# Kernel optimization log

Measured on AMD Instinct MI355X. Metric: run time of the kernel, lower is better.

The kernel has to match this reference:

```python
import jax, jax.numpy as jnp
import numpy as np

QMAX = 127.0  # int8 symmetric range


def _fake_quant(v, scale):
    # symmetric int8 fake-quantization with straight-through estimator
    q = jnp.round(jnp.clip(v / scale, -QMAX, QMAX)) * scale
    return v + jax.lax.stop_gradient(q - v)


def setup_inputs() -> dict:
    key = jax.random.key(0)
    k1, k2, k3 = jax.random.split(key, 3)
    B, S, Din, Dout = 4, 4096, 4096, 4096
    x = jax.random.normal(k1, (B, S, Din), dtype=jnp.float32)
    weight = jax.random.normal(k2, (Dout, Din), dtype=jnp.float32) * 0.02
    bias = jax.random.normal(k3, (Dout,), dtype=jnp.float32) * 0.02
    return {"x": x, "weight": weight, "bias": bias}


def reference(x, weight, bias):
    # per-tensor activation scale
    scale_x = jnp.maximum(jnp.max(jnp.abs(x)), 1e-8) / QMAX
    # per-output-channel weight scale: [Dout, 1]
    scale_w = jnp.maximum(jnp.max(jnp.abs(weight), axis=1, keepdims=True), 1e-8) / QMAX
    xq = _fake_quant(x, scale_x)
    wq = _fake_quant(weight, scale_w)
    # quantized linear: [B,S,Din] @ [Din,Dout] + bias
    return jnp.einsum('bsi,oi->bso', xq, wq) + bias
```

## Files before the change

kernel.cpp:

```cpp
#include <hip/hip_runtime.h>
#include <stdint.h>

#define QMAX_F 127.0f

typedef int    i32x4  __attribute__((ext_vector_type(4)));
typedef float  f32x4  __attribute__((ext_vector_type(4)));
typedef int8_t i8x16  __attribute__((ext_vector_type(16)));

#define GLOBAL_AS(p) ((const __attribute__((address_space(1))) void*)(p))
#define LDS_AS(p)    ((__attribute__((address_space(3))) void*)(p))

__global__ void init_ws_kernel(unsigned* absmax_bits) {
    if (threadIdx.x == 0) absmax_bits[0] = 0u;
}

__global__ void absmax_x_kernel(const float* __restrict__ x, size_t n4,
                                unsigned* __restrict__ out_bits) {
    size_t stride = (size_t)gridDim.x * blockDim.x;
    float m = 0.f;
    for (size_t i = (size_t)blockIdx.x * blockDim.x + threadIdx.x; i < n4; i += stride) {
        f32x4 v = reinterpret_cast<const f32x4*>(x)[i];
        m = fmaxf(m, fmaxf(fmaxf(fabsf(v[0]), fabsf(v[1])),
                           fmaxf(fabsf(v[2]), fabsf(v[3]))));
    }
    #pragma unroll
    for (int off = 32; off > 0; off >>= 1) m = fmaxf(m, __shfl_down(m, off));
    __shared__ float red[4];
    int lane = threadIdx.x & 63, wid = threadIdx.x >> 6;
    if (lane == 0) red[wid] = m;
    __syncthreads();
    if (threadIdx.x == 0) {
        m = fmaxf(fmaxf(red[0], red[1]), fmaxf(red[2], red[3]));
        atomicMax(out_bits, __float_as_uint(m));
    }
}

__global__ void rowmax_w_kernel(const float* __restrict__ w,
                                float* __restrict__ rowmax, int K) {
    int row = blockIdx.x;
    const f32x4* wr4 = reinterpret_cast<const f32x4*>(w + (size_t)row * K);
    float m = 0.f;
    for (int j = threadIdx.x; j < (K >> 2); j += blockDim.x) {
        f32x4 v = wr4[j];
        m = fmaxf(m, fmaxf(fmaxf(fabsf(v[0]), fabsf(v[1])),
                           fmaxf(fabsf(v[2]), fabsf(v[3]))));
    }
    #pragma unroll
    for (int off = 32; off > 0; off >>= 1) m = fmaxf(m, __shfl_down(m, off));
    __shared__ float red[4];
    int lane = threadIdx.x & 63, wid = threadIdx.x >> 6;
    if (lane == 0) red[wid] = m;
    __syncthreads();
    if (threadIdx.x == 0)
        rowmax[row] = fmaxf(fmaxf(red[0], red[1]), fmaxf(red[2], red[3]));
}

__global__ void quant_x_kernel(const float* __restrict__ x, int8_t* __restrict__ xq,
                               const unsigned* __restrict__ mx_bits, size_t n16) {
    float sx = fmaxf(__uint_as_float(*mx_bits), 1e-8f) / QMAX_F;
    size_t stride = (size_t)gridDim.x * blockDim.x;
    for (size_t i = (size_t)blockIdx.x * blockDim.x + threadIdx.x; i < n16; i += stride) {
        i8x16 q;
        #pragma unroll
        for (int j = 0; j < 4; ++j) {
            f32x4 v = reinterpret_cast<const f32x4*>(x)[i * 4 + j];
            #pragma unroll
            for (int k = 0; k < 4; ++k) {
                float t = fminf(fmaxf(v[k] / sx, -QMAX_F), QMAX_F);
                q[j * 4 + k] = (int8_t)__float2int_rn(t);
            }
        }
        reinterpret_cast<i8x16*>(xq)[i] = q;
    }
}

__global__ void quant_w_kernel(const float* __restrict__ w, int8_t* __restrict__ wq,
                               const float* __restrict__ rowmax,
                               float* __restrict__ scale_w, int K) {
    int row = blockIdx.x;
    float sw = fmaxf(rowmax[row], 1e-8f) / QMAX_F;
    if (threadIdx.x == 0) scale_w[row] = sw;
    const f32x4* src = reinterpret_cast<const f32x4*>(w + (size_t)row * K);
    int8_t* dst = wq + (size_t)row * K;
    for (int base = threadIdx.x * 16; base < K; base += blockDim.x * 16) {
        i8x16 q;
        #pragma unroll
        for (int j = 0; j < 4; ++j) {
            f32x4 v = src[(base >> 2) + j];
            #pragma unroll
            for (int k = 0; k < 4; ++k) {
                float t = fminf(fmaxf(v[k] / sw, -QMAX_F), QMAX_F);
                q[j * 4 + k] = (int8_t)__float2int_rn(t);
            }
        }
        *reinterpret_cast<i8x16*>(dst + base) = q;
    }
}

#define BM 128
#define BN 128
#define BKQ 64

__global__ __launch_bounds__(256) void gemm_i8_kernel(
        const int8_t* __restrict__ Aq, const int8_t* __restrict__ Bq,
        const unsigned* __restrict__ mx_bits, const float* __restrict__ scale_w,
        const float* __restrict__ bias, float* __restrict__ C,
        int M, int N, int K) {
    __shared__ __align__(16) int8_t lA[BM * BKQ];
    __shared__ __align__(16) int8_t lB[BN * BKQ];

    const int tid = threadIdx.x;
    const int l   = tid & 63;
    const int w   = tid >> 6;

    const int nwg = gridDim.x;
    const int wg  = (blockIdx.x & 7) * (nwg >> 3) + (blockIdx.x >> 3);
    const int tiles_n = N / BN;
    const int tm = wg / tiles_n, tn = wg % tiles_n;
    const size_t m0 = (size_t)tm * BM, n0 = (size_t)tn * BN;

    const int8_t* gA[2]; const int8_t* gB[2];
    const int8_t* ldsA[2]; const int8_t* ldsB[2];
    #pragma unroll
    for (int i = 0; i < 2; ++i) {
        int c   = w + 4 * i;
        int row = c * 16 + (l >> 2);
        int g   = (l & 3) ^ ((row >> 1) & 3);
        gA[i]   = Aq + (m0 + row) * (size_t)K + g * 16;
        gB[i]   = Bq + (n0 + row) * (size_t)K + g * 16;
        ldsA[i] = lA + c * 1024;
        ldsB[i] = lB + c * 1024;
    }

    const int wr = w >> 1, wc = w & 1;
    const int pbyte = (((l >> 4) ^ (((l & 15) >> 1) & 3)) << 4);
    int offA[4], offB[4];
    #pragma unroll
    for (int m = 0; m < 4; ++m) {
        offA[m] = (wr * 64 + m * 16 + (l & 15)) * BKQ + pbyte;
        offB[m] = (wc * 64 + m * 16 + (l & 15)) * BKQ + pbyte;
    }

    i32x4 acc[4][4];
    #pragma unroll
    for (int m = 0; m < 4; ++m)
        #pragma unroll
        for (int n = 0; n < 4; ++n)
            acc[m][n] = (i32x4){0, 0, 0, 0};

    for (int kt = 0; kt < K; kt += BKQ) {
        #pragma unroll
        for (int i = 0; i < 2; ++i) {
            __builtin_amdgcn_global_load_lds(GLOBAL_AS(gA[i] + kt), LDS_AS(ldsA[i]), 16, 0, 0);
            __builtin_amdgcn_global_load_lds(GLOBAL_AS(gB[i] + kt), LDS_AS(ldsB[i]), 16, 0, 0);
        }
        __syncthreads();

        i32x4 af[4], bf[4];
        #pragma unroll
        for (int m = 0; m < 4; ++m)
            af[m] = *reinterpret_cast<const i32x4*>(lA + offA[m]);
        #pragma unroll
        for (int n = 0; n < 4; ++n)
            bf[n] = *reinterpret_cast<const i32x4*>(lB + offB[n]);

        #pragma unroll
        for (int m = 0; m < 4; ++m)
            #pragma unroll
            for (int n = 0; n < 4; ++n)
                acc[m][n] = __builtin_amdgcn_mfma_i32_16x16x64_i8(af[m], bf[n], acc[m][n], 0, 0, 0);

        __syncthreads();
    }

    float sx = fmaxf(__uint_as_float(*mx_bits), 1e-8f) / QMAX_F;
    const int colb = (int)n0 + wc * 64 + (l & 15);
    const int rowb = (int)m0 + wr * 64 + ((l >> 4) << 2);
    #pragma unroll
    for (int n = 0; n < 4; ++n) {
        int col = colb + n * 16;
        float s  = sx * scale_w[col];
        float bv = bias[col];
        #pragma unroll
        for (int m = 0; m < 4; ++m) {
            size_t base = (size_t)(rowb + m * 16) * N + col;
            #pragma unroll
            for (int r = 0; r < 4; ++r)
                C[base + (size_t)r * N] = (float)acc[m][n][r] * s + bv;
        }
    }
}

extern "C" void kernel_launch(void* const* d_in, const int* in_sizes, int n_in,
                              void* d_out, int out_size, void* d_ws, size_t ws_size,
                              hipStream_t stream) {
    const float* x    = (const float*)d_in[0];
    const float* wt   = (const float*)d_in[1];
    const float* bias = (const float*)d_in[2];
    float* out        = (float*)d_out;

    const int N = in_sizes[2];
    const int K = in_sizes[1] / N;
    const int M = in_sizes[0] / K;
    const size_t nx = (size_t)in_sizes[0];
    const size_t nw = (size_t)in_sizes[1];

    uint8_t* ws = (uint8_t*)d_ws;
    unsigned* absmax_bits = (unsigned*)ws;
    float*    rowmax      = (float*)(ws + 1024);
    float*    scale_w     = (float*)(ws + 1024 + (size_t)N * 4 + 3072);
    int8_t*   xq          = (int8_t*)(ws + 65536);
    int8_t*   wq          = xq + nx;

    hipLaunchKernelGGL(init_ws_kernel, dim3(1), dim3(64), 0, stream, absmax_bits);
    hipLaunchKernelGGL(absmax_x_kernel, dim3(2048), dim3(256), 0, stream,
                       x, nx / 4, absmax_bits);
    hipLaunchKernelGGL(rowmax_w_kernel, dim3(N), dim3(256), 0, stream,
                       wt, rowmax, K);
    hipLaunchKernelGGL(quant_x_kernel, dim3(4096), dim3(256), 0, stream,
                       x, xq, absmax_bits, nx / 16);
    hipLaunchKernelGGL(quant_w_kernel, dim3(N), dim3(256), 0, stream,
                       wt, wq, rowmax, scale_w, K);

    dim3 ggrid((M / BM) * (N / BN));
    hipLaunchKernelGGL(gemm_i8_kernel, ggrid, dim3(256), 0, stream,
                       xq, wq, absmax_bits, scale_w, bias, out, M, N, K);
}
```

Before: 916.6 us.

## Rewrite int8 GEMM as double-buffered 256x256 tile pipeline and fuse weight quant

The int8 GEMM moves from 128x128 tiles with a single LDS buffer and a full barrier stall on each k-step to 256x256x128 tiles with 512 threads. It double-buffers LDS and interleaves async global-to-LDS loads with MFMA phases, using raised wave priority and partial vmcnt waits. The weight row-max and quantization kernels are merged into one pass that keeps each row in registers. The init kernel becomes a memset, and quantized outputs are packed into 32-bit words. The aim is to hide memory latency and raise arithmetic intensity, at the cost of more LDS and registers per block (launch_bounds 512,2) and a hardcoded assumption that K equals 4096 in the weight kernel.

```diff
diff --git a/kernel.cpp b/kernel.cpp
--- a/kernel.cpp
+++ b/kernel.cpp
@@ -3,16 +3,11 @@
 
 #define QMAX_F 127.0f
 
-typedef int    i32x4  __attribute__((ext_vector_type(4)));
-typedef float  f32x4  __attribute__((ext_vector_type(4)));
-typedef int8_t i8x16  __attribute__((ext_vector_type(16)));
+typedef int    i32x4 __attribute__((ext_vector_type(4)));
+typedef float  f32x4 __attribute__((ext_vector_type(4)));
 
 #define GLOBAL_AS(p) ((const __attribute__((address_space(1))) void*)(p))
 #define LDS_AS(p)    ((__attribute__((address_space(3))) void*)(p))
-
-__global__ void init_ws_kernel(unsigned* absmax_bits) {
-    if (threadIdx.x == 0) absmax_bits[0] = 0u;
-}
 
 __global__ void absmax_x_kernel(const float* __restrict__ x, size_t n4,
                                 unsigned* __restrict__ out_bits) {
@@ -35,83 +30,86 @@
     }
 }
 
-__global__ void rowmax_w_kernel(const float* __restrict__ w,
-                                float* __restrict__ rowmax, int K) {
-    int row = blockIdx.x;
-    const f32x4* wr4 = reinterpret_cast<const f32x4*>(w + (size_t)row * K);
-    float m = 0.f;
-    for (int j = threadIdx.x; j < (K >> 2); j += blockDim.x) {
-        f32x4 v = wr4[j];
-        m = fmaxf(m, fmaxf(fmaxf(fabsf(v[0]), fabsf(v[1])),
-                           fmaxf(fabsf(v[2]), fabsf(v[3]))));
-    }
-    #pragma unroll
-    for (int off = 32; off > 0; off >>= 1) m = fmaxf(m, __shfl_down(m, off));
-    __shared__ float red[4];
-    int lane = threadIdx.x & 63, wid = threadIdx.x >> 6;
-    if (lane == 0) red[wid] = m;
-    __syncthreads();
-    if (threadIdx.x == 0)
-        rowmax[row] = fmaxf(fmaxf(red[0], red[1]), fmaxf(red[2], red[3]));
-}
-
 __global__ void quant_x_kernel(const float* __restrict__ x, int8_t* __restrict__ xq,
                                const unsigned* __restrict__ mx_bits, size_t n16) {
     float sx = fmaxf(__uint_as_float(*mx_bits), 1e-8f) / QMAX_F;
     size_t stride = (size_t)gridDim.x * blockDim.x;
     for (size_t i = (size_t)blockIdx.x * blockDim.x + threadIdx.x; i < n16; i += stride) {
-        i8x16 q;
+        uint32_t q[4];
         #pragma unroll
         for (int j = 0; j < 4; ++j) {
             f32x4 v = reinterpret_cast<const f32x4*>(x)[i * 4 + j];
+            uint32_t p = 0;
             #pragma unroll
             for (int k = 0; k < 4; ++k) {
                 float t = fminf(fmaxf(v[k] / sx, -QMAX_F), QMAX_F);
-                q[j * 4 + k] = (int8_t)__float2int_rn(t);
+                p |= (uint32_t)(uint8_t)(int8_t)__float2int_rn(t) << (8 * k);
             }
+            q[j] = p;
         }
-        reinterpret_cast<i8x16*>(xq)[i] = q;
-    }
-}
-
-__global__ void quant_w_kernel(const float* __restrict__ w, int8_t* __restrict__ wq,
-                               const float* __restrict__ rowmax,
-                               float* __restrict__ scale_w, int K) {
+        reinterpret_cast<i32x4*>(xq)[i] =
+            (i32x4){(int)q[0], (int)q[1], (int)q[2], (int)q[3]};
+    }
+}
+
+__global__ __launch_bounds__(256) void wquant_kernel(const float* __restrict__ w,
+        int8_t* __restrict__ wq, float* __restrict__ scale_w, int K) {
     int row = blockIdx.x;
-    float sw = fmaxf(rowmax[row], 1e-8f) / QMAX_F;
-    if (threadIdx.x == 0) scale_w[row] = sw;
     const f32x4* src = reinterpret_cast<const f32x4*>(w + (size_t)row * K);
-    int8_t* dst = wq + (size_t)row * K;
-    for (int base = threadIdx.x * 16; base < K; base += blockDim.x * 16) {
-        i8x16 q;
+    f32x4 v[4];
+    float m = 0.f;
+    #pragma unroll
+    for (int j = 0; j < 4; ++j) {
+        v[j] = src[threadIdx.x + j * 256];
+        m = fmaxf(m, fmaxf(fmaxf(fabsf(v[j][0]), fabsf(v[j][1])),
+                           fmaxf(fabsf(v[j][2]), fabsf(v[j][3]))));
+    }
+    #pragma unroll
+    for (int off = 32; off > 0; off >>= 1) m = fmaxf(m, __shfl_down(m, off));
+    __shared__ float red[5];
+    int lane = threadIdx.x & 63, wid = threadIdx.x >> 6;
+    if (lane == 0) red[wid] = m;
+    __syncthreads();
+    if (threadIdx.x == 0) {
+        float mm = fmaxf(fmaxf(red[0], red[1]), fmaxf(red[2], red[3]));
+        float sw = fmaxf(mm, 1e-8f) / QMAX_F;
+        scale_w[row] = sw;
+        red[4] = sw;
+    }
+    __syncthreads();
+    float sw = red[4];
+    uint32_t* dst = reinterpret_cast<uint32_t*>(wq + (size_t)row * K);
+    #pragma unroll
+    for (int j = 0; j < 4; ++j) {
+        uint32_t p = 0;
         #pragma unroll
-        for (int j = 0; j < 4; ++j) {
-            f32x4 v = src[(base >> 2) + j];
-            #pragma unroll
-            for (int k = 0; k < 4; ++k) {
-                float t = fminf(fmaxf(v[k] / sw, -QMAX_F), QMAX_F);
-                q[j * 4 + k] = (int8_t)__float2int_rn(t);
-            }
+        for (int k = 0; k < 4; ++k) {
+            float t = fminf(fmaxf(v[j][k] / sw, -QMAX_F), QMAX_F);
+            p |= (uint32_t)(uint8_t)(int8_t)__float2int_rn(t) << (8 * k);
         }
-        *reinterpret_cast<i8x16*>(dst + base) = q;
-    }
-}
-
-#define BM 128
-#define BN 128
-#define BKQ 64
-
-__global__ __launch_bounds__(256) void gemm_i8_kernel(
+        dst[threadIdx.x + j * 256] = p;
+    }
+}
+
+#define BM 256
+#define BN 256
+#define BK 128
+
+#define LD128(p) (*reinterpret_cast<const i32x4*>(p))
+
+__global__ __launch_bounds__(512, 2) void gemm_i8_kernel(
         const int8_t* __restrict__ Aq, const int8_t* __restrict__ Bq,
         const unsigned* __restrict__ mx_bits, const float* __restrict__ scale_w,
         const float* __restrict__ bias, float* __restrict__ C,
         int M, int N, int K) {
-    __shared__ __align__(16) int8_t lA[BM * BKQ];
-    __shared__ __align__(16) int8_t lB[BN * BKQ];
+    __shared__ __align__(16) int8_t lA[2 * BM * BK];
+    __shared__ __align__(16) int8_t lB[2 * BN * BK];
 
     const int tid = threadIdx.x;
     const int l   = tid & 63;
     const int w   = tid >> 6;
+    const int wr  = w >> 2, wc = w & 3;
+    const int NT  = K / BK;
 
     const int nwg = gridDim.x;
     const int wg  = (blockIdx.x & 7) * (nwg >> 3) + (blockIdx.x >> 3);
@@ -119,71 +117,109 @@
     const int tm = wg / tiles_n, tn = wg % tiles_n;
     const size_t m0 = (size_t)tm * BM, n0 = (size_t)tn * BN;
 
-    const int8_t* gA[2]; const int8_t* gB[2];
-    const int8_t* ldsA[2]; const int8_t* ldsB[2];
-    #pragma unroll
-    for (int i = 0; i < 2; ++i) {
-        int c   = w + 4 * i;
-        int row = c * 16 + (l >> 2);
-        int g   = (l & 3) ^ ((row >> 1) & 3);
-        gA[i]   = Aq + (m0 + row) * (size_t)K + g * 16;
-        gB[i]   = Bq + (n0 + row) * (size_t)K + g * 16;
-        ldsA[i] = lA + c * 1024;
-        ldsB[i] = lB + c * 1024;
-    }
-
-    const int wr = w >> 1, wc = w & 1;
-    const int pbyte = (((l >> 4) ^ (((l & 15) >> 1) & 3)) << 4);
-    int offA[4], offB[4];
-    #pragma unroll
-    for (int m = 0; m < 4; ++m) {
-        offA[m] = (wr * 64 + m * 16 + (l & 15)) * BKQ + pbyte;
-        offB[m] = (wc * 64 + m * 16 + (l & 15)) * BKQ + pbyte;
-    }
-
-    i32x4 acc[4][4];
-    #pragma unroll
-    for (int m = 0; m < 4; ++m)
-        #pragma unroll
-        for (int n = 0; n < 4; ++n)
-            acc[m][n] = (i32x4){0, 0, 0, 0};
-
-    for (int kt = 0; kt < K; kt += BKQ) {
-        #pragma unroll
-        for (int i = 0; i < 2; ++i) {
-            __builtin_amdgcn_global_load_lds(GLOBAL_AS(gA[i] + kt), LDS_AS(ldsA[i]), 16, 0, 0);
-            __builtin_amdgcn_global_load_lds(GLOBAL_AS(gB[i] + kt), LDS_AS(ldsB[i]), 16, 0, 0);
-        }
-        __syncthreads();
-
-        i32x4 af[4], bf[4];
-        #pragma unroll
-        for (int m = 0; m < 4; ++m)
-            af[m] = *reinterpret_cast<const i32x4*>(lA + offA[m]);
-        #pragma unroll
-        for (int n = 0; n < 4; ++n)
-            bf[n] = *reinterpret_cast<const i32x4*>(lB + offB[n]);
-
-        #pragma unroll
-        for (int m = 0; m < 4; ++m)
-            #pragma unroll
-            for (int n = 0; n < 4; ++n)
-                acc[m][n] = __builtin_amdgcn_mfma_i32_16x16x64_i8(af[m], bf[n], acc[m][n], 0, 0, 0);
-
-        __syncthreads();
+    const int c0 = tid, c1 = 512 + tid;
+    const int srow0 = c0 >> 3, srow1 = c1 >> 3;
+    const int sgo0 = ((c0 & 7) ^ (srow0 & 7)) << 4;
+    const int sgo1 = ((c1 & 7) ^ (srow1 & 7)) << 4;
+    const size_t aoff0 = (m0 + srow0) * (size_t)K + sgo0;
+    const size_t aoff1 = (m0 + srow1) * (size_t)K + sgo1;
+    const size_t boff0 = (n0 + srow0) * (size_t)K + sgo0;
+    const size_t boff1 = (n0 + srow1) * (size_t)K + sgo1;
+    const int wbase = w * 1024;
+
+#define STAGE_A(buf, half, tile) do {                                              \
+    size_t t_ = (size_t)(((tile) < NT) ? (tile) : 0) * BK;                         \
+    __builtin_amdgcn_global_load_lds(                                              \
+        GLOBAL_AS(Aq + aoff0 + (size_t)(half) * 128 * K + t_),                     \
+        LDS_AS(lA + (buf) * 32768 + (half) * 16384 + wbase), 16, 0, 0);            \
+    __builtin_amdgcn_global_load_lds(                                              \
+        GLOBAL_AS(Aq + aoff1 + (size_t)(half) * 128 * K + t_),                     \
+        LDS_AS(lA + (buf) * 32768 + (half) * 16384 + 8192 + wbase), 16, 0, 0);     \
+} while (0)
+
+#define STAGE_B(buf, half, tile) do {                                              \
+    size_t t_ = (size_t)(((tile) < NT) ? (tile) : 0) * BK;                         \
+    __builtin_amdgcn_global_load_lds(                                              \
+        GLOBAL_AS(Bq + boff0 + (size_t)(half) * 128 * K + t_),                     \
+        LDS_AS(lB + (buf) * 32768 + (half) * 16384 + wbase), 16, 0, 0);            \
+    __builtin_amdgcn_global_load_lds(                                              \
+        GLOBAL_AS(Bq + boff1 + (size_t)(half) * 128 * K + t_),                     \
+        LDS_AS(lB + (buf) * 32768 + (half) * 16384 + 8192 + wbase), 16, 0, 0);     \
+} while (0)
+
+    const int arow = (wr * 128 + (l & 15)) * BK;
+    const int brow = (wc * 64  + (l & 15)) * BK;
+    const int sl0  = (((l >> 4)    ) ^ (l & 7)) << 4;
+    const int sl1  = (((l >> 4) + 4) ^ (l & 7)) << 4;
+#define SLOT(ks) ((ks) ? sl1 : sl0)
+
+    i32x4 acc[8][4] = {};
+    i32x4 bf[2][4];
+
+#define PHASE(buf, mh, ks, RB, STAGE_STMT, VMTAIL) do {                            \
+    const int8_t* Ab_ = lA + (buf) * 32768 + arow;                                 \
+    i32x4 a0_ = LD128(Ab_ + ((mh) * 4 + 0) * 2048 + SLOT(ks));                     \
+    i32x4 a1_ = LD128(Ab_ + ((mh) * 4 + 1) * 2048 + SLOT(ks));                     \
+    i32x4 a2_ = LD128(Ab_ + ((mh) * 4 + 2) * 2048 + SLOT(ks));                     \
+    i32x4 a3_ = LD128(Ab_ + ((mh) * 4 + 3) * 2048 + SLOT(ks));                     \
+    if ((RB) >= 0) {                                                               \
+        const int8_t* Bb_ = lB + (buf) * 32768 + brow;                             \
+        bf[(RB) & 1][0] = LD128(Bb_ + 0 * 2048 + SLOT((RB) & 1));                  \
+        bf[(RB) & 1][1] = LD128(Bb_ + 1 * 2048 + SLOT((RB) & 1));                  \
+        bf[(RB) & 1][2] = LD128(Bb_ + 2 * 2048 + SLOT((RB) & 1));                  \
+        bf[(RB) & 1][3] = LD128(Bb_ + 3 * 2048 + SLOT((RB) & 1));                  \
+    }                                                                              \
+    STAGE_STMT;                                                                    \
+    __builtin_amdgcn_s_barrier();                                                  \
+    asm volatile("s_waitcnt lgkmcnt(0)" ::: "memory");                             \
+    __builtin_amdgcn_s_setprio(1);                                                 \
+    _Pragma("unroll") for (int n_ = 0; n_ < 4; ++n_) {                             \
+        acc[(mh)*4+0][n_] = __builtin_amdgcn_mfma_i32_16x16x64_i8(a0_, bf[ks][n_], acc[(mh)*4+0][n_], 0, 0, 0); \
+        acc[(mh)*4+1][n_] = __builtin_amdgcn_mfma_i32_16x16x64_i8(a1_, bf[ks][n_], acc[(mh)*4+1][n_], 0, 0, 0); \
+        acc[(mh)*4+2][n_] = __builtin_amdgcn_mfma_i32_16x16x64_i8(a2_, bf[ks][n_], acc[(mh)*4+2][n_], 0, 0, 0); \
+        acc[(mh)*4+3][n_] = __builtin_amdgcn_mfma_i32_16x16x64_i8(a3_, bf[ks][n_], acc[(mh)*4+3][n_], 0, 0, 0); \
+    }                                                                              \
+    __builtin_amdgcn_s_setprio(0);                                                 \
+    VMTAIL;                                                                        \
+    __builtin_amdgcn_s_barrier();                                                  \
+    asm volatile("" ::: "memory");                                                 \
+} while (0)
+
+#define VMW4 asm volatile("s_waitcnt vmcnt(4)" ::: "memory")
+
+    STAGE_A(0, 0, 0); STAGE_A(0, 1, 0);
+    STAGE_B(0, 0, 0); STAGE_B(0, 1, 0);
+    STAGE_B(1, 0, 1); STAGE_B(1, 1, 1);
+    VMW4;
+    __builtin_amdgcn_s_barrier();
+    asm volatile("" ::: "memory");
+
+    #pragma unroll 1
+    for (int i = 0; i < NT / 2; ++i) {
+        const int t_a1 = 2 * i + 1;
+        const int t_n  = 2 * i + 2;
+        const int t_b3 = 2 * i + 3;
+        PHASE(0, 0, 0,  0, STAGE_A(1, 0, t_a1), );
+        PHASE(0, 1, 0,  1, STAGE_A(1, 1, t_a1), );
+        PHASE(0, 0, 1, -1, STAGE_B(0, 0, t_n),  );
+        PHASE(0, 1, 1, -1, STAGE_B(0, 1, t_n),  VMW4);
+        PHASE(1, 0, 0,  0, STAGE_A(0, 0, t_n),  );
+        PHASE(1, 1, 0,  1, STAGE_A(0, 1, t_n),  );
+        PHASE(1, 0, 1, -1, STAGE_B(1, 0, t_b3), );
+        PHASE(1, 1, 1, -1, STAGE_B(1, 1, t_b3), VMW4);
     }
 
     float sx = fmaxf(__uint_as_float(*mx_bits), 1e-8f) / QMAX_F;
-    const int colb = (int)n0 + wc * 64 + (l & 15);
-    const int rowb = (int)m0 + wr * 64 + ((l >> 4) << 2);
+    const int colb  = (int)n0 + wc * 64 + (l & 15);
+    const int rowb0 = (int)m0 + wr * 128 + ((l >> 4) << 2);
     #pragma unroll
     for (int n = 0; n < 4; ++n) {
-        int col = colb + n * 16;
+        int col  = colb + n * 16;
         float s  = sx * scale_w[col];
         float bv = bias[col];
         #pragma unroll
-        for (int m = 0; m < 4; ++m) {
-            size_t base = (size_t)(rowb + m * 16) * N + col;
+        for (int m = 0; m < 8; ++m) {
+            size_t base = (size_t)(rowb0 + m * 16) * N + col;
             #pragma unroll
             for (int r = 0; r < 4; ++r)
                 C[base + (size_t)r * N] = (float)acc[m][n][r] * s + bv;
@@ -207,22 +243,19 @@
 
     uint8_t* ws = (uint8_t*)d_ws;
     unsigned* absmax_bits = (unsigned*)ws;
-    float*    rowmax      = (float*)(ws + 1024);
-    float*    scale_w     = (float*)(ws + 1024 + (size_t)N * 4 + 3072);
+    float*    scale_w     = (float*)(ws + 4096);
     int8_t*   xq          = (int8_t*)(ws + 65536);
     int8_t*   wq          = xq + nx;
 
-    hipLaunchKernelGGL(init_ws_kernel, dim3(1), dim3(64), 0, stream, absmax_bits);
+    hipMemsetAsync(absmax_bits, 0, 4, stream);
     hipLaunchKernelGGL(absmax_x_kernel, dim3(2048), dim3(256), 0, stream,
                        x, nx / 4, absmax_bits);
-    hipLaunchKernelGGL(rowmax_w_kernel, dim3(N), dim3(256), 0, stream,
-                       wt, rowmax, K);
+    hipLaunchKernelGGL(wquant_kernel, dim3(N), dim3(256), 0, stream,
+                       wt, wq, scale_w, K);
     hipLaunchKernelGGL(quant_x_kernel, dim3(4096), dim3(256), 0, stream,
                        x, xq, absmax_bits, nx / 16);
-    hipLaunchKernelGGL(quant_w_kernel, dim3(N), dim3(256), 0, stream,
-                       wt, wq, rowmax, scale_w, K);
 
     dim3 ggrid((M / BM) * (N / BN));
-    hipLaunchKernelGGL(gemm_i8_kernel, ggrid, dim3(256), 0, stream,
+    hipLaunchKernelGGL(gemm_i8_kernel, ggrid, dim3(512), 0, stream,
                        xq, wq, absmax_bits, scale_w, bias, out, M, N, K);
 }
```

Measured after the change: 799.4 us. 12.8% less time.
